# Performance work log

Measured on AMD Instinct MI355X. Metric: run time of the kernel, lower is better.

## Reference

```python
import jax, jax.numpy as jnp
import numpy as np

N_NODES = 50000
N_EDGES = 400000
FEAT = 64      # irreps_in modeled as 64 scalar channels; head_dim == FEAT
HEADS = 4


def setup_inputs() -> dict:
    key = jax.random.key(0)
    k = jax.random.split(key, 7)
    x = jax.random.normal(k[0], (N_NODES, FEAT), dtype=jnp.float32)
    edge_index = jax.random.randint(k[1], (2, N_EDGES), 0, N_NODES, dtype=jnp.int32)
    s = 1.0 / np.sqrt(FEAT)
    Wq = jax.random.normal(k[2], (HEADS, FEAT, FEAT), dtype=jnp.float32) * s
    Wk = jax.random.normal(k[3], (HEADS, FEAT, FEAT), dtype=jnp.float32) * s
    Wv = jax.random.normal(k[4], (HEADS, FEAT, FEAT), dtype=jnp.float32) * s
    Wout = jax.random.normal(k[5], (FEAT, FEAT), dtype=jnp.float32) * s
    return {"x": x, "Wq": Wq, "Wk": Wk, "Wv": Wv, "Wout": Wout, "edge_index": edge_index}


def reference(x, Wq, Wk, Wv, Wout, edge_index):
    # Per-node attention over graph neighbors. The torch module pads neighbors
    # into degree buckets and runs SDPA per bucket; mathematically this is a
    # segment (per-receiver) softmax over incoming edges, which we compute
    # directly without padding or bucket loops.
    sender, receiver = edge_index[0], edge_index[1]
    n = x.shape[0]
    scale = x.shape[1] ** -0.5  # head_dim == FEAT in the original module

    Q = jnp.einsum('nf,hfd->hnd', x, Wq)  # (H, N, F)
    K = jnp.einsum('nf,hfd->hnd', x, Wk)
    V = jnp.einsum('nf,hfd->hnd', x, Wv)

    # Edge scores: q_receiver . k_sender per head -> (E, H)
    s = jnp.einsum('hef,hef->eh', Q[:, receiver], K[:, sender]) * scale

    # Numerically stable segment softmax over each receiver's neighborhood.
    m = jax.ops.segment_max(s, receiver, num_segments=n)          # (N, H)
    p = jnp.exp(s - m[receiver])                                   # (E, H)
    denom = jax.ops.segment_sum(p, receiver, num_segments=n)      # (N, H)
    alpha = p / denom[receiver]                                    # (E, H)

    # Weighted message aggregation: (H, E, F) scattered to (H, N, F).
    msg = alpha.T[:, :, None] * V[:, sender]
    agg = jax.vmap(lambda mh: jax.ops.segment_sum(mh, receiver, num_segments=n))(msg)

    out = jnp.nan_to_num(agg.mean(axis=0))  # deg-0 nodes contribute zeros
    return x + out @ Wout
```

## Files before the change

### kernel.cpp

```cpp
#include <hip/hip_runtime.h>

#define FEAT 64
#define HEADS 4
#define CAP 64
#define LROW 520
#define TSTR 80

typedef __attribute__((ext_vector_type(8))) short short8;
typedef __attribute__((ext_vector_type(8))) __bf16 bf16x8;
typedef __attribute__((ext_vector_type(4))) float floatx4;
typedef __attribute__((ext_vector_type(2))) float float2v;
typedef unsigned short ushortT;

static __device__ __forceinline__ unsigned short f2bf(float f) {
    union { float f; unsigned int u; } v; v.f = f;
    unsigned int u = v.u;
    u = u + 0x7fffu + ((u >> 16) & 1u);
    return (unsigned short)(u >> 16);
}
static __device__ __forceinline__ float bfl(unsigned int u) {
    union { unsigned int u; float f; } v; v.u = u << 16; return v.f;
}
static __device__ __forceinline__ float bfh(unsigned int u) {
    union { unsigned int u; float f; } v; v.u = u & 0xffff0000u; return v.f;
}

template <int CTRL>
static __device__ __forceinline__ float dppadd(float v) {
    int y = __builtin_amdgcn_update_dpp(0, __builtin_bit_cast(int, v),
                                        CTRL, 0xf, 0xf, true);
    return v + __builtin_bit_cast(float, y);
}

__global__ __launch_bounds__(256) void k_init(const float* __restrict__ Wq,
        const float* __restrict__ Wk, const float* __restrict__ Wv,
        const float* __restrict__ Wout, short8* __restrict__ Wpack,
        short8* __restrict__ WoutPack, int4* __restrict__ deg4, int nslots) {
    int t = blockIdx.x * 256 + threadIdx.x;
    if (t < nslots) deg4[t] = make_int4(0, 0, 0, 0);
    int o = t;
    if (o < 12 * 2 * 4 * 64) {
        int lane = o & 63, dt = (o >> 6) & 3, kb = (o >> 8) & 1, m = o >> 9;
        int mat = m >> 2, h = m & 3;
        const float* src = (mat == 0) ? Wq : (mat == 1) ? Wk : Wv;
        src += (size_t)h * 64 * 64;
        int d = dt * 16 + (lane & 15);
        int kbase = kb * 32 + (lane >> 4) * 8;
        short8 val;
#pragma unroll
        for (int j = 0; j < 8; j++)
            val[j] = (short)f2bf(src[(kbase + j) * 64 + d]);
        Wpack[o] = val;
    } else if (o < 6144 + 512) {
        int idx = o - 6144;
        int lane = idx & 63, kb = (idx >> 6) & 1, nt = idx >> 7;
        int d = nt * 16 + (lane & 15);
        int kbase = kb * 32 + (lane >> 4) * 8;
        short8 val;
#pragma unroll
        for (int j = 0; j < 8; j++)
            val[j] = (short)f2bf(Wout[(kbase + j) * 64 + d]);
        WoutPack[idx] = val;
    }
}

__global__ __launch_bounds__(256) void k_qkv(const float* __restrict__ x,
        const short8* __restrict__ Wpack, const int* __restrict__ send,
        const int* __restrict__ recv, int* __restrict__ deg,
        int* __restrict__ srt, ushortT* __restrict__ Qb, ushortT* __restrict__ KVb,
        int E) {
    __shared__ ushortT lds[16 * LROW];
    int w = threadIdx.x >> 6, lane = threadIdx.x & 63;
    int quad = lane >> 4, lrow = lane & 15;
    int ntile = blockIdx.x * 16;
    const float* xrow = x + (size_t)(ntile + lrow) * 64 + quad * 8;
    float4 fa = *(const float4*)(xrow);
    float4 fb = *(const float4*)(xrow + 4);
    float4 fc = *(const float4*)(xrow + 32);
    float4 fd = *(const float4*)(xrow + 36);
    short8 a0 = {(short)f2bf(fa.x), (short)f2bf(fa.y), (short)f2bf(fa.z), (short)f2bf(fa.w),
                 (short)f2bf(fb.x), (short)f2bf(fb.y), (short)f2bf(fb.z), (short)f2bf(fb.w)};
    short8 a1 = {(short)f2bf(fc.x), (short)f2bf(fc.y), (short)f2bf(fc.z), (short)f2bf(fc.w),
                 (short)f2bf(fd.x), (short)f2bf(fd.y), (short)f2bf(fd.z), (short)f2bf(fd.w)};
    bf16x8 X0 = __builtin_bit_cast(bf16x8, a0);
    bf16x8 X1 = __builtin_bit_cast(bf16x8, a1);
#pragma unroll
    for (int mat = 0; mat < 3; mat++) {
        int m = mat * 4 + w;
#pragma unroll
        for (int dt = 0; dt < 4; dt++) {
            floatx4 acc = {0.f, 0.f, 0.f, 0.f};
            short8 b0 = Wpack[((m * 2 + 0) * 4 + dt) * 64 + lane];
            short8 b1 = Wpack[((m * 2 + 1) * 4 + dt) * 64 + lane];
            acc = __builtin_amdgcn_mfma_f32_16x16x32_bf16(
                __builtin_bit_cast(bf16x8, b0), X0, acc, 0, 0, 0);
            acc = __builtin_amdgcn_mfma_f32_16x16x32_bf16(
                __builtin_bit_cast(bf16x8, b1), X1, acc, 0, 0, 0);
            if (mat == 0) {
                unsigned int u01 = (unsigned)f2bf(acc[0] * 0.125f)
                                 | ((unsigned)f2bf(acc[1] * 0.125f) << 16);
                unsigned int u23 = (unsigned)f2bf(acc[2] * 0.125f)
                                 | ((unsigned)f2bf(acc[3] * 0.125f) << 16);
                *(uint2*)&lds[lrow * LROW + w * 64 + dt * 16 + quad * 4]
                    = make_uint2(u01, u23);
            } else {
                int p = __builtin_amdgcn_cvt_pk_fp8_f32(acc[0], acc[1], 0, false);
                p = __builtin_amdgcn_cvt_pk_fp8_f32(acc[2], acc[3], p, true);
                int slot = w * 16 + dt * 4 + quad;
                *(unsigned int*)&lds[lrow * LROW + 256 + slot * 4 + ((mat == 2) ? 2 : 0)]
                    = (unsigned int)p;
            }
        }
    }
    __syncthreads();
    {
        int u = threadIdx.x;
#pragma unroll
        for (int rep = 0; rep < 2; rep++, u += 256) {
            int row = u >> 5, idx = u & 31;
            uint4 val = *(const uint4*)&lds[row * LROW + idx * 8];
            *(uint4*)(Qb + ((size_t)(ntile + row)) * 256 + idx * 8) = val;
        }
    }
    {
        uint4* KVq = (uint4*)KVb;
        int u = threadIdx.x;
#pragma unroll
        for (int rep = 0; rep < 2; rep++, u += 256) {
            int row = u >> 5, idx = u & 31;
            uint4 val = *(const uint4*)&lds[row * LROW + 256 + idx * 8];
            KVq[(size_t)(ntile + row) * 32 + idx] = val;
        }
    }
    int e = blockIdx.x * 256 + threadIdx.x;
    if (e < E) {
        int r = recv[e];
        int pos = atomicAdd(&deg[r], 1);
        if (pos < CAP) srt[(size_t)r * CAP + pos] = send[e];
    }
}

__global__ __launch_bounds__(256) void k_attn(const ushortT* __restrict__ Qb,
        const ushortT* __restrict__ KVb, const short8* __restrict__ WoutPack,
        const int* __restrict__ deg, const int* __restrict__ srt,
        const float* __restrict__ x, float* __restrict__ out, int N) {
    __shared__ ushortT tl[16 * TSTR];
    int w = threadIdx.x >> 6, lane = threadIdx.x & 63;
    int el = lane & 31, e_sel = lane >> 5, jj = lane & 7;
    int rb = blockIdx.x * 16;
    const uint4* KV4 = (const uint4*)KVb;

    for (int rr = 0; rr < 4; rr++) {
        int ridx = w * 4 + rr;
        int r = rb + ridx;
        uint4 qu = ((const uint4*)(Qb + (size_t)r * 256))[el];
        float2v q01 = {bfl(qu.x), bfh(qu.x)};
        float2v q23 = {bfl(qu.y), bfh(qu.y)};
        float2v q45 = {bfl(qu.z), bfh(qu.z)};
        float2v q67 = {bfl(qu.w), bfh(qu.w)};
        float2v acc01 = {0.f, 0.f}, acc23 = {0.f, 0.f};
        float2v acc45 = {0.f, 0.f}, acc67 = {0.f, 0.f};
        float den = 0.f;
        const int* myslots = srt + (size_t)r * CAP;
        int d = min(deg[r], CAP);

#define PROC2(kv, pmask)                                                  \
    {                                                                     \
        float2v kA = __builtin_amdgcn_cvt_pk_f32_fp8(kv.x, false);        \
        float2v kB = __builtin_amdgcn_cvt_pk_f32_fp8(kv.x, true);         \
        float2v kC = __builtin_amdgcn_cvt_pk_f32_fp8(kv.z, false);        \
        float2v kD = __builtin_amdgcn_cvt_pk_f32_fp8(kv.z, true);         \
        float2v d2 = q01 * kA;                                            \
        d2 += q23 * kB;                                                   \
        d2 += q45 * kC;                                                   \
        d2 += q67 * kD;                                                   \
        float sp = d2.x + d2.y;                                           \
        sp = dppadd<0xB1>(sp);                                            \
        sp = dppadd<0x4E>(sp);                                            \
        sp = dppadd<0x141>(sp);                                           \
        float p = __expf(sp);                                             \
        p = (pmask) ? p : 0.f;                                            \
        float2v vA = __builtin_amdgcn_cvt_pk_f32_fp8(kv.y, false);        \
        float2v vB = __builtin_amdgcn_cvt_pk_f32_fp8(kv.y, true);         \
        float2v vC = __builtin_amdgcn_cvt_pk_f32_fp8(kv.w, false);        \
        float2v vD = __builtin_amdgcn_cvt_pk_f32_fp8(kv.w, true);         \
        float2v pp = {p, p};                                              \
        den += p;                                                         \
        acc01 += pp * vA; acc23 += pp * vB;                               \
        acc45 += pp * vC; acc67 += pp * vD;                               \
    }
        int i = 0;
        for (; i + 7 < d; i += 8) {
            int4 sa = *(const int4*)(myslots + i);
            int4 sb = *(const int4*)(myslots + i + 4);
            int s0 = e_sel ? sa.y : sa.x;
            int s1 = e_sel ? sa.w : sa.z;
            int s2 = e_sel ? sb.y : sb.x;
            int s3 = e_sel ? sb.w : sb.z;
            uint4 kv0 = KV4[(size_t)s0 * 32 + el];
            uint4 kv1 = KV4[(size_t)s1 * 32 + el];
            uint4 kv2 = KV4[(size_t)s2 * 32 + el];
            uint4 kv3 = KV4[(size_t)s3 * 32 + el];
            PROC2(kv0, true) PROC2(kv1, true) PROC2(kv2, true) PROC2(kv3, true)
        }
        if (i + 3 < d) {
            int4 s4 = *(const int4*)(myslots + i);
            int s01 = e_sel ? s4.y : s4.x;
            int s23 = e_sel ? s4.w : s4.z;
            uint4 kv0 = KV4[(size_t)s01 * 32 + el];
            uint4 kv1 = KV4[(size_t)s23 * 32 + el];
            PROC2(kv0, true) PROC2(kv1, true)
            i += 4;
        }
        for (; i < d; i += 2) {
            int idx = i + e_sel;
            int slot = myslots[min(idx, d - 1)];
            uint4 kv = KV4[(size_t)slot * 32 + el];
            PROC2(kv, idx < d)
        }
#undef PROC2
        float a0 = acc01.x, a1 = acc01.y, a2 = acc23.x, a3 = acc23.y;
        float a4 = acc45.x, a5 = acc45.y, a6 = acc67.x, a7 = acc67.y;
        den += __shfl_xor(den, 32);
        a0 += __shfl_xor(a0, 32); a1 += __shfl_xor(a1, 32);
        a2 += __shfl_xor(a2, 32); a3 += __shfl_xor(a3, 32);
        a4 += __shfl_xor(a4, 32); a5 += __shfl_xor(a5, 32);
        a6 += __shfl_xor(a6, 32); a7 += __shfl_xor(a7, 32);
        float inv = (den > 0.f) ? 0.25f / den : 0.f;
        a0 *= inv; a1 *= inv; a2 *= inv; a3 *= inv;
        a4 *= inv; a5 *= inv; a6 *= inv; a7 *= inv;
        a0 = dppadd<0x128>(a0); a1 = dppadd<0x128>(a1);
        a2 = dppadd<0x128>(a2); a3 = dppadd<0x128>(a3);
        a4 = dppadd<0x128>(a4); a5 = dppadd<0x128>(a5);
        a6 = dppadd<0x128>(a6); a7 = dppadd<0x128>(a7);
        a0 += __shfl_xor(a0, 16); a1 += __shfl_xor(a1, 16);
        a2 += __shfl_xor(a2, 16); a3 += __shfl_xor(a3, 16);
        a4 += __shfl_xor(a4, 16); a5 += __shfl_xor(a5, 16);
        a6 += __shfl_xor(a6, 16); a7 += __shfl_xor(a7, 16);
        if (lane < 8) {
            uint4 tv;
            tv.x = (unsigned)f2bf(a0) | ((unsigned)f2bf(a1) << 16);
            tv.y = (unsigned)f2bf(a2) | ((unsigned)f2bf(a3) << 16);
            tv.z = (unsigned)f2bf(a4) | ((unsigned)f2bf(a5) << 16);
            tv.w = (unsigned)f2bf(a6) | ((unsigned)f2bf(a7) << 16);
            *(uint4*)&tl[ridx * TSTR + jj * 8] = tv;
        }
    }
    __syncthreads();

    int q = lane >> 4, c = lane & 15;
    short8 ta0 = *(const short8*)&tl[c * TSTR + q * 8];
    short8 ta1 = *(const short8*)&tl[c * TSTR + 32 + q * 8];
    short8 tb0 = WoutPack[(w * 2 + 0) * 64 + lane];
    short8 tb1 = WoutPack[(w * 2 + 1) * 64 + lane];
    floatx4 acc = {0.f, 0.f, 0.f, 0.f};
    acc = __builtin_amdgcn_mfma_f32_16x16x32_bf16(
        __builtin_bit_cast(bf16x8, ta0), __builtin_bit_cast(bf16x8, tb0), acc, 0, 0, 0);
    acc = __builtin_amdgcn_mfma_f32_16x16x32_bf16(
        __builtin_bit_cast(bf16x8, ta1), __builtin_bit_cast(bf16x8, tb1), acc, 0, 0, 0);
#pragma unroll
    for (int reg = 0; reg < 4; reg++) {
        size_t idx = (size_t)(rb + q * 4 + reg) * 64 + w * 16 + c;
        out[idx] = x[idx] + acc[reg];
    }
}

extern "C" void kernel_launch(void* const* d_in, const int* in_sizes, int n_in,
                              void* d_out, int out_size, void* d_ws, size_t ws_size,
                              hipStream_t stream) {
    const float* x    = (const float*)d_in[0];
    const float* Wq   = (const float*)d_in[1];
    const float* Wk   = (const float*)d_in[2];
    const float* Wv   = (const float*)d_in[3];
    const float* Wout = (const float*)d_in[4];
    const int*   ei   = (const int*)d_in[5];
    int N = in_sizes[0] / FEAT;
    int E = in_sizes[5] / 2;
    const int* send = ei;
    const int* recv = ei + E;

    char* ws = (char*)d_ws;
    size_t o = 0;
    auto alloc = [&](size_t bytes) {
        void* p = ws + o;
        o = (o + bytes + 255) & ~(size_t)255;
        return p;
    };
    ushortT* Qb      = (ushortT*)alloc((size_t)N * 256 * 2);
    ushortT* KVb     = (ushortT*)alloc((size_t)N * 512);
    short8* Wpack    = (short8*)alloc(6144 * sizeof(short8));
    short8* WoutPack = (short8*)alloc(512 * sizeof(short8));
    int* deg         = (int*)alloc((size_t)((N + 3) & ~3) * 4);
    int* srt         = (int*)alloc((size_t)N * CAP * 4);

    int nslots = ((N + 3) & ~3) / 4;
    k_init<<<64, 256, 0, stream>>>(Wq, Wk, Wv, Wout, Wpack, WoutPack,
                                   (int4*)deg, nslots);
    k_qkv<<<N / 16, 256, 0, stream>>>(x, Wpack, send, recv, deg, srt, Qb, KVb, E);
    k_attn<<<N / 16, 256, 0, stream>>>(Qb, KVb, WoutPack, deg, srt, x,
                                       (float*)d_out, N);
}
```

Baseline: 149.9 us.

## Process two receivers per wave half and prefetch first eight neighbor rows

The attention kernel now gives each half-wave its own receiver node instead of splitting one receiver's edges across halves, which removes the cross-half reduction shuffles. Degrees, Q rows and the first eight slot indices for both receiver pairs are loaded up front, and the first eight K/V gathers are issued unconditionally (masked indices point to node 0) to expose memory parallelism. In the QKV kernel, the edge atomicAdd and index loads are moved before the matmul so their latency overlaps it. The risk is wasted gathers for low-degree nodes and higher register pressure.

Measured after the change: 141.3 us. -5.8%, faster.

```diff
diff --git a/kernel.cpp b/kernel.cpp
--- a/kernel.cpp
+++ b/kernel.cpp
@@ -73,6 +73,15 @@
     int w = threadIdx.x >> 6, lane = threadIdx.x & 63;
     int quad = lane >> 4, lrow = lane & 15;
     int ntile = blockIdx.x * 16;
+
+    int e = blockIdx.x * 256 + threadIdx.x;
+    int r_edge = 0, s_edge = 0, pos = CAP;
+    if (e < E) {
+        r_edge = recv[e];
+        s_edge = send[e];
+        pos = atomicAdd(&deg[r_edge], 1);
+    }
+
     const float* xrow = x + (size_t)(ntile + lrow) * 64 + quad * 8;
     float4 fa = *(const float4*)(xrow);
     float4 fb = *(const float4*)(xrow + 4);
@@ -132,12 +141,7 @@
             KVq[(size_t)(ntile + row) * 32 + idx] = val;
         }
     }
-    int e = blockIdx.x * 256 + threadIdx.x;
-    if (e < E) {
-        int r = recv[e];
-        int pos = atomicAdd(&deg[r], 1);
-        if (pos < CAP) srt[(size_t)r * CAP + pos] = send[e];
-    }
+    if (e < E && pos < CAP) srt[(size_t)r_edge * CAP + pos] = s_edge;
 }
 
 __global__ __launch_bounds__(256) void k_attn(const ushortT* __restrict__ Qb,
@@ -146,14 +150,41 @@
         const float* __restrict__ x, float* __restrict__ out, int N) {
     __shared__ ushortT tl[16 * TSTR];
     int w = threadIdx.x >> 6, lane = threadIdx.x & 63;
-    int el = lane & 31, e_sel = lane >> 5, jj = lane & 7;
+    int hs = lane >> 5, hl = lane & 31, jj = hl & 7;
     int rb = blockIdx.x * 16;
     const uint4* KV4 = (const uint4*)KVb;
 
-    for (int rr = 0; rr < 4; rr++) {
-        int ridx = w * 4 + rr;
-        int r = rb + ridx;
-        uint4 qu = ((const uint4*)(Qb + (size_t)r * 256))[el];
+    int d_[2]; uint4 qu_[2]; int4 sf_[2], s2_[2]; const int* slots_[2];
+#pragma unroll
+    for (int p = 0; p < 2; p++) {
+        int r = rb + w * 4 + p * 2 + hs;
+        d_[p] = min(deg[r], CAP);
+        slots_[p] = srt + (size_t)r * CAP;
+        qu_[p] = ((const uint4*)(Qb + (size_t)r * 256))[hl];
+        sf_[p] = *(const int4*)(slots_[p]);
+        s2_[p] = *(const int4*)(slots_[p] + 4);
+    }
+
+#pragma unroll
+    for (int p = 0; p < 2; p++) {
+        int d = d_[p];
+        int s0 = (0 < d) ? sf_[p].x : 0;
+        int s1 = (1 < d) ? sf_[p].y : 0;
+        int s2v = (2 < d) ? sf_[p].z : 0;
+        int s3 = (3 < d) ? sf_[p].w : 0;
+        int s4v = (4 < d) ? s2_[p].x : 0;
+        int s5 = (5 < d) ? s2_[p].y : 0;
+        int s6 = (6 < d) ? s2_[p].z : 0;
+        int s7 = (7 < d) ? s2_[p].w : 0;
+        uint4 kv0 = KV4[(size_t)s0 * 32 + hl];
+        uint4 kv1 = KV4[(size_t)s1 * 32 + hl];
+        uint4 kv2 = KV4[(size_t)s2v * 32 + hl];
+        uint4 kv3 = KV4[(size_t)s3 * 32 + hl];
+        uint4 kv4 = KV4[(size_t)s4v * 32 + hl];
+        uint4 kv5 = KV4[(size_t)s5 * 32 + hl];
+        uint4 kv6 = KV4[(size_t)s6 * 32 + hl];
+        uint4 kv7 = KV4[(size_t)s7 * 32 + hl];
+        uint4 qu = qu_[p];
         float2v q01 = {bfl(qu.x), bfh(qu.x)};
         float2v q23 = {bfl(qu.y), bfh(qu.y)};
         float2v q45 = {bfl(qu.z), bfh(qu.z)};
@@ -161,10 +192,8 @@
         float2v acc01 = {0.f, 0.f}, acc23 = {0.f, 0.f};
         float2v acc45 = {0.f, 0.f}, acc67 = {0.f, 0.f};
         float den = 0.f;
-        const int* myslots = srt + (size_t)r * CAP;
-        int d = min(deg[r], CAP);
-
-#define PROC2(kv, pmask)                                                  \
+
+#define PROC(kv, pmask)                                                   \
     {                                                                     \
         float2v kA = __builtin_amdgcn_cvt_pk_f32_fp8(kv.x, false);        \
         float2v kB = __builtin_amdgcn_cvt_pk_f32_fp8(kv.x, true);         \
@@ -178,54 +207,35 @@
         sp = dppadd<0xB1>(sp);                                            \
         sp = dppadd<0x4E>(sp);                                            \
         sp = dppadd<0x141>(sp);                                           \
-        float p = __expf(sp);                                             \
-        p = (pmask) ? p : 0.f;                                            \
+        float pv = __expf(sp);                                            \
+        pv = (pmask) ? pv : 0.f;                                          \
         float2v vA = __builtin_amdgcn_cvt_pk_f32_fp8(kv.y, false);        \
         float2v vB = __builtin_amdgcn_cvt_pk_f32_fp8(kv.y, true);         \
         float2v vC = __builtin_amdgcn_cvt_pk_f32_fp8(kv.w, false);        \
         float2v vD = __builtin_amdgcn_cvt_pk_f32_fp8(kv.w, true);         \
-        float2v pp = {p, p};                                              \
-        den += p;                                                         \
+        float2v pp = {pv, pv};                                            \
+        den += pv;                                                        \
         acc01 += pp * vA; acc23 += pp * vB;                               \
         acc45 += pp * vC; acc67 += pp * vD;                               \
     }
-        int i = 0;
-        for (; i + 7 < d; i += 8) {
-            int4 sa = *(const int4*)(myslots + i);
-            int4 sb = *(const int4*)(myslots + i + 4);
-            int s0 = e_sel ? sa.y : sa.x;
-            int s1 = e_sel ? sa.w : sa.z;
-            int s2 = e_sel ? sb.y : sb.x;
-            int s3 = e_sel ? sb.w : sb.z;
-            uint4 kv0 = KV4[(size_t)s0 * 32 + el];
-            uint4 kv1 = KV4[(size_t)s1 * 32 + el];
-            uint4 kv2 = KV4[(size_t)s2 * 32 + el];
-            uint4 kv3 = KV4[(size_t)s3 * 32 + el];
-            PROC2(kv0, true) PROC2(kv1, true) PROC2(kv2, true) PROC2(kv3, true)
-        }
-        if (i + 3 < d) {
-            int4 s4 = *(const int4*)(myslots + i);
-            int s01 = e_sel ? s4.y : s4.x;
-            int s23 = e_sel ? s4.w : s4.z;
-            uint4 kv0 = KV4[(size_t)s01 * 32 + el];
-            uint4 kv1 = KV4[(size_t)s23 * 32 + el];
-            PROC2(kv0, true) PROC2(kv1, true)
-            i += 4;
-        }
-        for (; i < d; i += 2) {
-            int idx = i + e_sel;
-            int slot = myslots[min(idx, d - 1)];
-            uint4 kv = KV4[(size_t)slot * 32 + el];
-            PROC2(kv, idx < d)
-        }
-#undef PROC2
+        PROC(kv0, 0 < d) PROC(kv1, 1 < d) PROC(kv2, 2 < d) PROC(kv3, 3 < d)
+        PROC(kv4, 4 < d) PROC(kv5, 5 < d) PROC(kv6, 6 < d) PROC(kv7, 7 < d)
+
+        for (int i = 8; i < d; i += 4) {
+            int4 s4 = *(const int4*)(slots_[p] + i);
+            int t0 = s4.x;
+            int t1 = (i + 1 < d) ? s4.y : 0;
+            int t2 = (i + 2 < d) ? s4.z : 0;
+            int t3 = (i + 3 < d) ? s4.w : 0;
+            uint4 ka = KV4[(size_t)t0 * 32 + hl];
+            uint4 kb = KV4[(size_t)t1 * 32 + hl];
+            uint4 kc = KV4[(size_t)t2 * 32 + hl];
+            uint4 kd = KV4[(size_t)t3 * 32 + hl];
+            PROC(ka, true) PROC(kb, i + 1 < d) PROC(kc, i + 2 < d) PROC(kd, i + 3 < d)
+        }
+#undef PROC
         float a0 = acc01.x, a1 = acc01.y, a2 = acc23.x, a3 = acc23.y;
         float a4 = acc45.x, a5 = acc45.y, a6 = acc67.x, a7 = acc67.y;
-        den += __shfl_xor(den, 32);
-        a0 += __shfl_xor(a0, 32); a1 += __shfl_xor(a1, 32);
-        a2 += __shfl_xor(a2, 32); a3 += __shfl_xor(a3, 32);
-        a4 += __shfl_xor(a4, 32); a5 += __shfl_xor(a5, 32);
-        a6 += __shfl_xor(a6, 32); a7 += __shfl_xor(a7, 32);
         float inv = (den > 0.f) ? 0.25f / den : 0.f;
         a0 *= inv; a1 *= inv; a2 *= inv; a3 *= inv;
         a4 *= inv; a5 *= inv; a6 *= inv; a7 *= inv;
@@ -237,7 +247,8 @@
         a2 += __shfl_xor(a2, 16); a3 += __shfl_xor(a3, 16);
         a4 += __shfl_xor(a4, 16); a5 += __shfl_xor(a5, 16);
         a6 += __shfl_xor(a6, 16); a7 += __shfl_xor(a7, 16);
-        if (lane < 8) {
+        if (hl < 8) {
+            int ridx = w * 4 + p * 2 + hs;
             uint4 tv;
             tv.x = (unsigned)f2bf(a0) | ((unsigned)f2bf(a1) << 16);
             tv.y = (unsigned)f2bf(a2) | ((unsigned)f2bf(a3) << 16);
```
